# Kernel optimization log

Hardware: AMD Instinct MI355X
Metric: run time of the kernel (lower is better)

Reference implementation:

```python
import jax, jax.numpy as jnp
import numpy as np

J = 24       # num_joints
DIM = 3      # point dim
CD = 128     # c_dim
BN = 4       # bottleneck_size
HPG = 32     # hidden per group (hidden_size=768 / 24)

def setup_inputs() -> dict:
    key = jax.random.key(0)
    ks = jax.random.split(key, 16)
    B, T = 4, 25000
    s = lambda k, shape, fan_in: jax.random.normal(k, shape, jnp.float32) * (1.0 / np.sqrt(fan_in))
    return {
        "p": jax.random.normal(ks[0], (B, J * DIM, T), jnp.float32),
        "z": jax.random.normal(ks[1], (B, 128), jnp.float32),
        "c": jax.random.normal(ks[2], (B, CD), jnp.float32),
        # grouped Conv1d weights stored as (J, out_per_group, in_per_group)
        "W_proj": s(ks[3], (J, BN, CD), CD),          "b_proj": jnp.zeros((J * BN,), jnp.float32),
        "W_p":   s(ks[4], (J, HPG, DIM + BN), DIM+BN), "b_p":   jnp.zeros((J * HPG,), jnp.float32),
        "W0":    s(ks[5], (J, HPG, HPG), HPG),         "b0":    jnp.zeros((J * HPG,), jnp.float32),
        "W1":    s(ks[6], (J, HPG, HPG), HPG),         "b1":    jnp.zeros((J * HPG,), jnp.float32),
        "W2":    s(ks[7], (J, HPG, HPG), HPG),         "b2":    jnp.zeros((J * HPG,), jnp.float32),
        "W_out": s(ks[8], (J, 1, HPG), HPG),           "b_out": jnp.zeros((J,), jnp.float32),
    }

def _gconv(x, W, b):
    # grouped 1x1 conv: x (B,J,Cin,T), W (J,Cout,Cin), b (J*Cout,) -> (B,J,Cout,T)
    y = jnp.einsum('bjit,joi->bjot', x, W)
    return y + b.reshape(1, J, -1, 1)

def reference(p, z, c, W_proj, b_proj, W_p, b_p, W0, b0, W1, b1, W2, b2, W_out, b_out):
    B, _, T = p.shape
    # p.view(B, J, -1, T) then keep last `dim` channels
    p_in = p.reshape(B, J, -1, T)[:, :, -DIM:, :]            # (B,J,3,T)
    # 2D c branch: repeat per joint, grouped proj, broadcast over T
    c_rep = jnp.broadcast_to(c[:, None, :], (B, J, CD))       # (B,J,128)
    c_proj = jnp.einsum('bjc,joc->bjo', c_rep, W_proj) + b_proj.reshape(1, J, BN)
    c_proj = jnp.broadcast_to(c_proj[:, :, :, None], (B, J, BN, T))
    x = jnp.concatenate([p_in, c_proj], axis=2)               # (B,J,3+4,T)
    net = jax.nn.relu(_gconv(x,   W_p, b_p))
    net = jax.nn.relu(_gconv(net, W0,  b0))
    net = jax.nn.relu(_gconv(net, W1,  b1))
    net = jax.nn.relu(_gconv(net, W2,  b2))
    out = _gconv(net, W_out, b_out)                           # (B,J,1,T)
    return out.reshape(B, J, T)                               # logits (B, num_joints, T)
```

## Files before the change

### kernel.cpp

```cpp
#include <hip/hip_runtime.h>
#include <hip/hip_bf16.h>

#define NJ 24
#define TLEN 25000
#define NB 4
#define CHUNKS 20
#define NWPB (CHUNKS*4)
#define NIT32 ((TLEN+31)/32)

typedef short short8 __attribute__((ext_vector_type(8)));
typedef short s16x2 __attribute__((ext_vector_type(2)));
typedef float f32x16 __attribute__((ext_vector_type(16)));

union FragU { unsigned u[4]; short8 s; };

__device__ __forceinline__ unsigned pack2(float a, float b){
    unsigned ua = __float_as_uint(a) + 0x8000u;
    unsigned ub = __float_as_uint(b) + 0x8000u;
    return __builtin_amdgcn_perm(ub, ua, 0x07060302u);
}
__device__ __forceinline__ float bflo(unsigned u){
    union { unsigned v; float f; } t; t.v = u << 16; return t.f;
}

__device__ __forceinline__ unsigned pkrelu(unsigned x){
    union { unsigned u; s16x2 v; } a, r;
    a.u = x;
    s16x2 z; z[0] = 0; z[1] = 0;
    r.v = __builtin_elementwise_max(a.v, z);
    return r.u;
}

__device__ __forceinline__ f32x16 mfma(const FragU &a, const FragU &b, f32x16 c){
    return __builtin_amdgcn_mfma_f32_32x32x16_bf16(a.s, b.s, c, 0, 0, 0);
}

__device__ __forceinline__ FragU mk1(unsigned w){
    FragU f; f.u[0] = w; f.u[1] = 0; f.u[2] = 0; f.u[3] = 0; return f;
}

__device__ __forceinline__ void relu_pack(const f32x16 &acc, FragU &k0, FragU &k1){
    unsigned w[8];
    #pragma unroll
    for (int i = 0; i < 8; ++i) w[i] = pkrelu(pack2(acc[2*i], acc[2*i+1]));
    k0.u[0]=w[0]; k0.u[1]=w[1]; k0.u[2]=w[2]; k0.u[3]=w[3];
    k1.u[0]=w[4]; k1.u[1]=w[5]; k1.u[2]=w[6]; k1.u[3]=w[7];
}

__global__ __launch_bounds__(256, 2) void ptf_decoder_kernel(
    const float* __restrict__ p,    const float* __restrict__ c,
    const float* __restrict__ Wproj,const float* __restrict__ bproj,
    const float* __restrict__ Wp,   const float* __restrict__ bp,
    const float* __restrict__ W0,   const float* __restrict__ b0,
    const float* __restrict__ W1,   const float* __restrict__ b1,
    const float* __restrict__ W2,   const float* __restrict__ b2,
    const float* __restrict__ Wout, const float* __restrict__ bout,
    float* __restrict__ out)
{
    __shared__ __align__(16) float ldsW[3][32][36];
    __shared__ __align__(16) float ldsWp[32][8];
    __shared__ __align__(16) float ldsB[3][32];
    __shared__ __align__(16) float ldsWo[32];

    const int tid = threadIdx.x;
    const int bj  = blockIdx.x % (NB*NJ);
    const int sub = blockIdx.x / (NB*NJ);
    const int b   = bj / NJ;
    const int j   = bj % NJ;

    {
        const float* Wl[3] = {W0, W1, W2};
        #pragma unroll
        for (int L = 0; L < 3; ++L) {
            int row = tid >> 3, c4 = tid & 7;
            float4 v = *reinterpret_cast<const float4*>(Wl[L] + ((size_t)(j*32 + row))*32 + c4*4);
            *reinterpret_cast<float4*>(&ldsW[L][row][c4*4]) = v;
        }
        {
            int row = tid >> 3, i8 = tid & 7;
            ldsWp[row][i8] = (i8 < 7) ? Wp[((size_t)(j*32 + row))*7 + i8]
                                      : bp[j*32 + row];
        }
        if      (tid < 32)  ldsB[0][tid]      = b0[j*32 + tid];
        else if (tid < 64)  ldsB[1][tid-32]   = b1[j*32 + tid-32];
        else if (tid < 96)  ldsB[2][tid-64]   = b2[j*32 + tid-64];
        else if (tid < 128) ldsWo[tid-96]     = Wout[j*32 + tid-96];
    }
    __syncthreads();

    const int lane = tid & 63;
    const int row  = lane & 31;
    const int h    = lane >> 5;

    FragU whi[3][2];
    #pragma unroll
    for (int L = 0; L < 3; ++L) {
        #pragma unroll
        for (int kh = 0; kh < 2; ++kh) {
            const int g  = kh*2 + h;
            const int cA = (g >> 1)*4 + (g & 1);
            const float* base = &ldsW[L][row][0];
            float4 x = *reinterpret_cast<const float4*>(base + cA*4);
            float4 y = *reinterpret_cast<const float4*>(base + (cA+2)*4);
            whi[L][kh].u[0] = pack2(x.x, x.y);
            whi[L][kh].u[1] = pack2(x.z, x.w);
            whi[L][kh].u[2] = pack2(y.x, y.y);
            whi[L][kh].u[3] = pack2(y.z, y.w);
        }
    }
    FragU woF[2];
    #pragma unroll
    for (int kh = 0; kh < 2; ++kh) {
        const int g  = kh*2 + h;
        const int cA = (g >> 1)*4 + (g & 1);
        float4 x = *reinterpret_cast<const float4*>(&ldsWo[cA*4]);
        float4 y = *reinterpret_cast<const float4*>(&ldsWo[(cA+2)*4]);
        woF[kh].u[0] = pack2(x.x, x.y);
        woF[kh].u[1] = pack2(x.z, x.w);
        woF[kh].u[2] = pack2(y.x, y.y);
        woF[kh].u[3] = pack2(y.z, y.w);
    }
    FragU wphi;
    {
        float4 x = make_float4(0,0,0,0), y = make_float4(0,0,0,0);
        if (lane < 32) {
            x = *reinterpret_cast<const float4*>(&ldsWp[row][0]);
            y = *reinterpret_cast<const float4*>(&ldsWp[row][4]);
        }
        wphi.u[0] = pack2(x.x, x.y);
        wphi.u[1] = pack2(x.z, x.w);
        wphi.u[2] = pack2(y.x, y.y);
        wphi.u[3] = pack2(y.z, y.w);
    }

    unsigned biasA[3];
    #pragma unroll
    for (int L = 0; L < 3; ++L) {
        float bl = (h == 0) ? ldsB[L][row] : 0.f;
        unsigned t = pack2(bl, 0.f);
        float res = bl - bflo(t);
        biasA[L] = (h == 0) ? pack2(bl, res) : 0u;
    }
    const unsigned ones2 = (h == 0) ? 0x3f803f80u : 0u;

    f32x16 kZero;
    #pragma unroll
    for (int r = 0; r < 16; ++r) kZero[r] = 0.f;

    float cacc0, cacc1, cacc2, cacc3;
    {
        const float* cb  = c + (size_t)b*128;
        const float* wpj = Wproj + (size_t)j*4*128;
        float cl = cb[lane], chv = cb[lane + 64];
        cacc0 = cl*wpj[0*128+lane] + chv*wpj[0*128+lane+64];
        cacc1 = cl*wpj[1*128+lane] + chv*wpj[1*128+lane+64];
        cacc2 = cl*wpj[2*128+lane] + chv*wpj[2*128+lane+64];
        cacc3 = cl*wpj[3*128+lane] + chv*wpj[3*128+lane+64];
        #pragma unroll
        for (int off = 32; off >= 1; off >>= 1) {
            cacc0 += __shfl_xor(cacc0, off, 64);
            cacc1 += __shfl_xor(cacc1, off, 64);
            cacc2 += __shfl_xor(cacc2, off, 64);
            cacc3 += __shfl_xor(cacc3, off, 64);
        }
        cacc0 += bproj[j*4+0]; cacc1 += bproj[j*4+1];
        cacc2 += bproj[j*4+2]; cacc3 += bproj[j*4+3];
    }
    const float c0v = (lane < 32) ? cacc0 : 0.f;
    unsigned wc2h = pack2(cacc1, cacc2);
    unsigned wc3h = pack2(cacc3, 1.0f);
    if (lane >= 32) { wc2h = 0; wc3h = 0; }
    const float bo = bout[j];

    const float* pb0 = p + ((size_t)(b*(NJ*3) + j*3 + 0))*TLEN;
    const float* pb1 = pb0 + TLEN;
    const float* pb2 = pb1 + TLEN;
    float* ob = out + ((size_t)(b*NJ + j))*TLEN;

    const int w0idx = sub*4 + (tid >> 6);

    auto loadP = [&](int itx, float&x0, float&x1, float&x2){
        x0=0.f; x1=0.f; x2=0.f;
        if (itx < NIT32 && lane < 32) {
            int t = itx*32 + lane;
            t = t < TLEN ? t : TLEN-1;
            x0 = pb0[t]; x1 = pb1[t]; x2 = pb2[t];
        }
    };

    float a0,a1,a2;
    loadP(w0idx, a0,a1,a2);

    for (int it = w0idx; it < NIT32; it += NWPB) {
        float n0,n1,n2;
        loadP(it + NWPB, n0,n1,n2);

        FragU fh;
        fh.u[0] = pack2(a0, a1);
        fh.u[1] = pack2(a2, c0v);
        fh.u[2] = wc2h;
        fh.u[3] = wc3h;

        f32x16 acc = mfma(wphi, fh, kZero);

        #pragma unroll
        for (int L = 0; L < 3; ++L) {
            f32x16 bAcc = mfma(mk1(biasA[L]), mk1(ones2), kZero);
            FragU p0, p1;
            relu_pack(acc, p0, p1);
            acc = mfma(whi[L][0], p0, bAcc);
            acc = mfma(whi[L][1], p1, acc);
        }

        FragU q0, q1;
        relu_pack(acc, q0, q1);
        f32x16 o = mfma(woF[0], q0, kZero);
        o = mfma(woF[1], q1, o);

        int t = it*32 + row;
        if (lane < 32 && t < TLEN) ob[t] = o[0] + bo;

        a0=n0; a1=n1; a2=n2;
    }
}

extern "C" void kernel_launch(void* const* d_in, const int* in_sizes, int n_in,
                              void* d_out, int out_size, void* d_ws, size_t ws_size,
                              hipStream_t stream) {
    const float* p     = (const float*)d_in[0];
    const float* c     = (const float*)d_in[2];
    const float* Wproj = (const float*)d_in[3];
    const float* bproj = (const float*)d_in[4];
    const float* Wp    = (const float*)d_in[5];
    const float* bp    = (const float*)d_in[6];
    const float* W0    = (const float*)d_in[7];
    const float* b0    = (const float*)d_in[8];
    const float* W1    = (const float*)d_in[9];
    const float* b1    = (const float*)d_in[10];
    const float* W2    = (const float*)d_in[11];
    const float* b2    = (const float*)d_in[12];
    const float* Wout  = (const float*)d_in[13];
    const float* bout  = (const float*)d_in[14];
    float* out = (float*)d_out;

    dim3 grid(NB*NJ*CHUNKS), block(256);
    ptf_decoder_kernel<<<grid, block, 0, stream>>>(
        p, c, Wproj, bproj, Wp, bp, W0, b0, W1, b1, W2, b2, Wout, bout, out);
}
```

Baseline: 38.50 us.

## Process four timesteps per lane with float4 loads and stores

Each lane now loads float4 vectors of the three point channels and runs four independent MFMA layer chains per loop iteration, one per timestep. Results are written back as a single float4 store. The grid shrinks from 20 to 7 chunks per (batch, joint) to match the coarser work unit. The goal is fewer, wider memory transactions and more independent MFMA work in flight to hide dependency latency. The cost is higher register pressure and a smaller grid, which may not fill the GPU evenly.

```diff
diff --git a/kernel.cpp b/kernel.cpp
--- a/kernel.cpp
+++ b/kernel.cpp
@@ -4,9 +4,9 @@
 #define NJ 24
 #define TLEN 25000
 #define NB 4
-#define CHUNKS 20
+#define CHUNKS 7
 #define NWPB (CHUNKS*4)
-#define NIT32 ((TLEN+31)/32)
+#define NGRP ((TLEN+127)/128)
 
 typedef short short8 __attribute__((ext_vector_type(8)));
 typedef short s16x2 __attribute__((ext_vector_type(2)));
@@ -179,48 +179,65 @@
 
     const int w0idx = sub*4 + (tid >> 6);
 
-    auto loadP = [&](int itx, float&x0, float&x1, float&x2){
-        x0=0.f; x1=0.f; x2=0.f;
-        if (itx < NIT32 && lane < 32) {
-            int t = itx*32 + lane;
-            t = t < TLEN ? t : TLEN-1;
-            x0 = pb0[t]; x1 = pb1[t]; x2 = pb2[t];
+    auto loadG = [&](int gx, float4&x0, float4&x1, float4&x2){
+        x0 = make_float4(0,0,0,0);
+        x1 = make_float4(0,0,0,0);
+        x2 = make_float4(0,0,0,0);
+        gx = gx < NGRP ? gx : NGRP-1;
+        int t = gx*128 + row*4;
+        t = (t + 3 < TLEN) ? t : (TLEN - 4);
+        if (lane < 32) {
+            x0 = *reinterpret_cast<const float4*>(pb0 + t);
+            x1 = *reinterpret_cast<const float4*>(pb1 + t);
+            x2 = *reinterpret_cast<const float4*>(pb2 + t);
         }
     };
 
-    float a0,a1,a2;
-    loadP(w0idx, a0,a1,a2);
-
-    for (int it = w0idx; it < NIT32; it += NWPB) {
-        float n0,n1,n2;
-        loadP(it + NWPB, n0,n1,n2);
-
-        FragU fh;
-        fh.u[0] = pack2(a0, a1);
-        fh.u[1] = pack2(a2, c0v);
-        fh.u[2] = wc2h;
-        fh.u[3] = wc3h;
-
-        f32x16 acc = mfma(wphi, fh, kZero);
-
-        #pragma unroll
-        for (int L = 0; L < 3; ++L) {
-            f32x16 bAcc = mfma(mk1(biasA[L]), mk1(ones2), kZero);
-            FragU p0, p1;
-            relu_pack(acc, p0, p1);
-            acc = mfma(whi[L][0], p0, bAcc);
-            acc = mfma(whi[L][1], p1, acc);
-        }
-
-        FragU q0, q1;
-        relu_pack(acc, q0, q1);
-        f32x16 o = mfma(woF[0], q0, kZero);
-        o = mfma(woF[1], q1, o);
-
-        int t = it*32 + row;
-        if (lane < 32 && t < TLEN) ob[t] = o[0] + bo;
-
-        a0=n0; a1=n1; a2=n2;
+    float4 A0, A1, A2;
+    loadG(w0idx, A0, A1, A2);
+
+    for (int g = w0idx; g < NGRP; g += NWPB) {
+        float4 N0, N1, N2;
+        loadG(g + NWPB, N0, N1, N2);
+
+        float ov[4];
+        const float Ax[4] = {A0.x, A0.y, A0.z, A0.w};
+        const float Ay[4] = {A1.x, A1.y, A1.z, A1.w};
+        const float Az[4] = {A2.x, A2.y, A2.z, A2.w};
+
+        #pragma unroll
+        for (int k = 0; k < 4; ++k) {
+            FragU fh;
+            fh.u[0] = pack2(Ax[k], Ay[k]);
+            fh.u[1] = pack2(Az[k], c0v);
+            fh.u[2] = wc2h;
+            fh.u[3] = wc3h;
+
+            f32x16 acc = mfma(wphi, fh, kZero);
+
+            #pragma unroll
+            for (int L = 0; L < 3; ++L) {
+                f32x16 bAcc = mfma(mk1(biasA[L]), mk1(ones2), kZero);
+                FragU p0, p1;
+                relu_pack(acc, p0, p1);
+                acc = mfma(whi[L][0], p0, bAcc);
+                acc = mfma(whi[L][1], p1, acc);
+            }
+
+            FragU q0, q1;
+            relu_pack(acc, q0, q1);
+            f32x16 o = mfma(woF[0], q0, kZero);
+            o = mfma(woF[1], q1, o);
+            ov[k] = o[0] + bo;
+        }
+
+        int t0 = g*128 + row*4;
+        if (lane < 32 && t0 + 3 < TLEN) {
+            float4 o4 = make_float4(ov[0], ov[1], ov[2], ov[3]);
+            *reinterpret_cast<float4*>(ob + t0) = o4;
+        }
+
+        A0 = N0; A1 = N1; A2 = N2;
     }
 }
 
```

Measured after the change: 37.39 us. -2.9%, faster.
